# Performance work log

Hardware: AMD Instinct MI355X
Metric: run time of the kernel (lower is better)

## Reference

```python
import jax, jax.numpy as jnp
import numpy as np


def setup_inputs() -> dict:
    key = jax.random.key(0)
    kx, ka = jax.random.split(key)
    B, N, F = 8, 2048, 64
    x = jax.random.normal(kx, (B, N, F), dtype=jnp.float32)
    a = jax.random.uniform(ka, (B, N, N), dtype=jnp.float32)  # adjacency weights in [0,1)
    return {"x": x, "a": a}


def reference(x, a):
    # t[b,i,f] = sum_j a[b,i,j] * x[b,j,f]
    t = jnp.einsum("bij,bjf->bif", a, x)
    # MAX/IND: 1.0 where aggregated signal exceeds 0.5, else 0.0
    # (faithful to tf.where(t>0.5, t/t, t*0.0))
    out = jnp.where(t > 0.5, t / t, t * 0.0)
    return out
```

## Files before the change

kernel.cpp:

```cpp
#include <hip/hip_runtime.h>

#define BATCH 8
#define NROW  2048
#define NF    64
#define JSPLIT 4
#define JPB   (NROW / JSPLIT)
#define CHUNK 32
#define TOT   ((size_t)BATCH * NROW * NF)

typedef float  f32x4  __attribute__((ext_vector_type(4)));
typedef __bf16 bf16x8 __attribute__((ext_vector_type(8)));
typedef unsigned short u16x8 __attribute__((ext_vector_type(8)));

union frag_cast { u16x8 u; bf16x8 b; };

#define AS1 __attribute__((address_space(1)))
#define AS3 __attribute__((address_space(3)))

__device__ __forceinline__ void gld16f(const float* g, float* l) {
  __builtin_amdgcn_global_load_lds((const AS1 void*)g, (AS3 void*)l, 16, 0, 0);
}
__device__ __forceinline__ void gld16u(const unsigned short* g, unsigned short* l) {
  __builtin_amdgcn_global_load_lds((const AS1 void*)g, (AS3 void*)l, 16, 0, 0);
}
__device__ __forceinline__ float ubits(unsigned u) {
  union { unsigned u; float f; } c; c.u = u; return c.f;
}
__device__ __forceinline__ unsigned fbits(float f) {
  union { float f; unsigned u; } c; c.f = f; return c.u;
}

__global__ __launch_bounds__(256, 4)
void prep_x(const float* __restrict__ xg, unsigned short* __restrict__ xs) {
  __shared__ float t[64][65];
  const int b  = blockIdx.y;
  const int j0 = blockIdx.x * 64;
  const int l  = threadIdx.x & 63;
  const int g  = threadIdx.x >> 6;
  const float* src = xg + ((size_t)b * NROW + j0) * NF;
#pragma unroll
  for (int k = 0; k < 16; ++k) {
    const int j = g * 16 + k;
    t[j][l] = src[(size_t)j * NF + l];
  }
  __syncthreads();
#pragma unroll
  for (int k = 0; k < 16; ++k) {
    const int f = g * 16 + k;
    const float v = t[l][f];
    const unsigned u0 = fbits(v);
    const float f0 = ubits(u0 & 0xFFFF0000u);
    const float r  = v - f0;
    const unsigned u1 = fbits(r);
    const float f1 = ubits(u1 & 0xFFFF0000u);
    const float r2 = r - f1;
    const unsigned u2 = fbits(r2);
    const unsigned short s2 =
        (unsigned short)((u2 + 0x7FFFu + ((u2 >> 16) & 1u)) >> 16);
    const size_t o = ((size_t)b * NF + f) * NROW + j0 + l;
    xs[o]           = (unsigned short)(u0 >> 16);
    xs[o + TOT]     = (unsigned short)(u1 >> 16);
    xs[o + 2 * TOT] = s2;
  }
}

__device__ __forceinline__ void split8(const f32x4 q0, const f32x4 q1,
                                       frag_cast* Af) {
  float av[8];
  *(f32x4*)&av[0] = q0;
  *(f32x4*)&av[4] = q1;
  u16x8 h0, h1, h2;
#pragma unroll
  for (int e = 0; e < 8; ++e) {
    const unsigned u0 = fbits(av[e]);
    const float f0 = ubits(u0 & 0xFFFF0000u);
    const float r  = av[e] - f0;
    const unsigned u1 = fbits(r);
    const float f1 = ubits(u1 & 0xFFFF0000u);
    const float r2 = r - f1;
    const unsigned u2 = fbits(r2);
    h0[e] = (unsigned short)(u0 >> 16);
    h1[e] = (unsigned short)(u1 >> 16);
    h2[e] = (unsigned short)((u2 + 0x7FFFu + ((u2 >> 16) & 1u)) >> 16);
  }
  Af[0].u = h0; Af[1].u = h1; Af[2].u = h2;
}

template <bool DIRECT>
__global__ __launch_bounds__(256, 4)
void gemm_mfma(const float* __restrict__ ag, const unsigned short* __restrict__ xs,
               float* __restrict__ outg, float* __restrict__ wp) {
  __shared__ __align__(16) float sA[2][64 * CHUNK];
  __shared__ __align__(16) unsigned short sB[2][3 * 64 * CHUNK];

  const int tid  = threadIdx.x;
  const int ln   = tid & 63;
  const int wv   = tid >> 6;
  const int ln15 = ln & 15;
  const int g    = ln >> 4;
  const int akey = ln15 & 7;
  const int bkey = (ln15 >> 1) & 3;

  const int nwg = gridDim.x * gridDim.y * gridDim.z;
  int flat = blockIdx.x + gridDim.x * (blockIdx.y + gridDim.y * blockIdx.z);
  flat = (flat & 7) * (nwg >> 3) + (flat >> 3);
  const int bx   = flat & 31;
  const int rest = flat >> 5;
  const int z    = DIRECT ? 0 : (rest & 3);
  const int b    = DIRECT ? rest : (rest >> 2);

  const int i0  = bx * 64;
  const int jb  = z * JPB;
  const int nch = (DIRECT ? NROW : JPB) / CHUNK;

  const float* aB = ag + ((size_t)b * NROW + i0) * NROW;
  const unsigned short* xB = xs + (size_t)b * NF * NROW;

  auto stage = [&](int buf, int j0) {
#pragma unroll
    for (int r = 0; r < 2; ++r) {
      const int s   = r * 256 + tid;
      const int row = s >> 3;
      const int q   = (s & 7) ^ (row & 7);
      gld16f(aB + (size_t)row * NROW + j0 + q * 4,
             &sA[buf][0] + (r * 256 + wv * 64) * 4);
    }
#pragma unroll
    for (int lvl = 0; lvl < 3; ++lvl) {
      const int n = tid >> 2;
      const int q = (tid & 3) ^ ((n >> 1) & 3);
      gld16u(xB + (size_t)lvl * TOT + (size_t)n * NROW + j0 + q * 8,
             &sB[buf][0] + (lvl * 256 + wv * 64) * 8);
    }
  };

  double macc[4][4];
#pragma unroll
  for (int i = 0; i < 4; ++i)
#pragma unroll
    for (int j = 0; j < 4; ++j) macc[i][j] = 0.0;

  constexpr int AI[6] = {2, 0, 1, 1, 0, 0};
  constexpr int BI[6] = {0, 2, 1, 0, 1, 0};

  stage(0, jb);

#pragma unroll 1
  for (int t = 0; t < nch; ++t) {
    __syncthreads();
    if (t + 1 < nch) stage((t + 1) & 1, jb + (t + 1) * CHUNK);

    const float* sAb = &sA[t & 1][0];
    const unsigned short* sBb = &sB[t & 1][0];

    const int rowOff = (wv * 16 + ln15) * 32;
    const f32x4 q0 = *(const f32x4*)(sAb + rowOff + (((2 * g)     ^ akey) << 2));
    const f32x4 q1 = *(const f32x4*)(sAb + rowOff + (((2 * g + 1) ^ akey) << 2));
    frag_cast Af[3];
    split8(q0, q1, Af);

    const int bpos = (g ^ bkey) * 8;
    f32x4 c[4];
#pragma unroll
    for (int nt = 0; nt < 4; ++nt) c[nt] = (f32x4){0.f, 0.f, 0.f, 0.f};

#pragma unroll
    for (int ng = 0; ng < 2; ++ng) {
      frag_cast Bv[2][3];
#pragma unroll
      for (int nn = 0; nn < 2; ++nn)
#pragma unroll
        for (int lvl = 0; lvl < 3; ++lvl)
          Bv[nn][lvl].u = *(const u16x8*)(
              sBb + lvl * 2048 + ((ng * 2 + nn) * 16 + ln15) * 32 + bpos);
#pragma unroll
      for (int term = 0; term < 6; ++term)
#pragma unroll
        for (int nn = 0; nn < 2; ++nn) {
          const int nt = ng * 2 + nn;
          c[nt] = __builtin_amdgcn_mfma_f32_16x16x32_bf16(
              Af[AI[term]].b, Bv[nn][BI[term]].b, c[nt], 0, 0, 0);
        }
    }
#pragma unroll
    for (int nt = 0; nt < 4; ++nt) {
      macc[nt][0] += (double)c[nt].x;
      macc[nt][1] += (double)c[nt].y;
      macc[nt][2] += (double)c[nt].z;
      macc[nt][3] += (double)c[nt].w;
    }
  }

  if (DIRECT) {
#pragma unroll
    for (int nt = 0; nt < 4; ++nt)
#pragma unroll
      for (int r = 0; r < 4; ++r)
        outg[((size_t)b * NROW + i0 + wv * 16 + g * 4 + r) * NF + nt * 16 + ln15] =
            (macc[nt][r] > 0.5) ? 1.0f : 0.0f;
  } else {
    float* wb = wp + (size_t)z * TOT;
#pragma unroll
    for (int nt = 0; nt < 4; ++nt)
#pragma unroll
      for (int r = 0; r < 4; ++r)
        wb[((size_t)b * NROW + i0 + wv * 16 + g * 4 + r) * NF + nt * 16 + ln15] =
            (float)macc[nt][r];
  }
}

__global__ __launch_bounds__(256)
void combine_thresh(const float* __restrict__ wsv, float* __restrict__ outg) {
  const size_t e = ((size_t)blockIdx.x * 256 + threadIdx.x) * 4;
  f32x4 p0 = *(const f32x4*)(wsv + e);
  f32x4 p1 = *(const f32x4*)(wsv + e + TOT);
  f32x4 p2 = *(const f32x4*)(wsv + e + 2 * TOT);
  f32x4 p3 = *(const f32x4*)(wsv + e + 3 * TOT);
  f32x4 o;
  o.x = (((double)p0.x + p1.x + p2.x + p3.x) > 0.5) ? 1.0f : 0.0f;
  o.y = (((double)p0.y + p1.y + p2.y + p3.y) > 0.5) ? 1.0f : 0.0f;
  o.z = (((double)p0.z + p1.z + p2.z + p3.z) > 0.5) ? 1.0f : 0.0f;
  o.w = (((double)p0.w + p1.w + p2.w + p3.w) > 0.5) ? 1.0f : 0.0f;
  *(f32x4*)(outg + e) = o;
}

extern "C" void kernel_launch(void* const* d_in, const int* in_sizes, int n_in,
                              void* d_out, int out_size, void* d_ws, size_t ws_size,
                              hipStream_t stream) {
  const float* x = (const float*)d_in[0];
  const float* a = (const float*)d_in[1];
  float* out = (float*)d_out;
  unsigned short* xs = (unsigned short*)d_ws;
  float* wp = (float*)((char*)d_ws + 3 * TOT * sizeof(unsigned short));

  prep_x<<<dim3(NROW / 64, BATCH), dim3(256), 0, stream>>>(x, xs);

  const size_t need = 3 * TOT * sizeof(unsigned short)
                    + (size_t)JSPLIT * TOT * sizeof(float);
  if (ws_size >= need) {
    gemm_mfma<false><<<dim3(NROW / 64, JSPLIT, BATCH), dim3(256), 0, stream>>>(
        a, xs, out, wp);
    combine_thresh<<<dim3((unsigned)(TOT / 1024)), dim3(256), 0, stream>>>(wp, out);
  } else {
    gemm_mfma<true><<<dim3(NROW / 64, 1, BATCH), dim3(256), 0, stream>>>(
        a, xs, out, nullptr);
  }
}
```

Baseline: 47.85 us.

## Switch to 32x32x16 MFMA tiles with 2x2 wave split and flat batch-major grid

```diff
diff --git a/kernel.cpp b/kernel.cpp
--- a/kernel.cpp
+++ b/kernel.cpp
@@ -9,6 +9,7 @@
 #define TOT   ((size_t)BATCH * NROW * NF)
 
 typedef float  f32x4  __attribute__((ext_vector_type(4)));
+typedef float  f32x16 __attribute__((ext_vector_type(16)));
 typedef __bf16 bf16x8 __attribute__((ext_vector_type(8)));
 typedef unsigned short u16x8 __attribute__((ext_vector_type(8)));
 
@@ -93,37 +94,33 @@
   __shared__ __align__(16) float sA[2][64 * CHUNK];
   __shared__ __align__(16) unsigned short sB[2][3 * 64 * CHUNK];
 
-  const int tid  = threadIdx.x;
-  const int ln   = tid & 63;
-  const int wv   = tid >> 6;
-  const int ln15 = ln & 15;
-  const int g    = ln >> 4;
-  const int akey = ln15 & 7;
-  const int bkey = (ln15 >> 1) & 3;
-
-  const int nwg = gridDim.x * gridDim.y * gridDim.z;
-  int flat = blockIdx.x + gridDim.x * (blockIdx.y + gridDim.y * blockIdx.z);
-  flat = (flat & 7) * (nwg >> 3) + (flat >> 3);
-  const int bx   = flat & 31;
-  const int rest = flat >> 5;
-  const int z    = DIRECT ? 0 : (rest & 3);
-  const int b    = DIRECT ? rest : (rest >> 2);
-
-  const int i0  = bx * 64;
-  const int jb  = z * JPB;
-  const int nch = (DIRECT ? NROW : JPB) / CHUNK;
+  const int tid   = threadIdx.x;
+  const int ln    = tid & 63;
+  const int wv    = tid >> 6;
+  const int l31   = ln & 31;
+  const int h     = ln >> 5;
+  const int rhalf = wv & 1;
+  const int chalf = wv >> 1;
+
+  const int flat = blockIdx.x;
+  const int b    = flat & 7;
+  const int bx   = (flat >> 3) & 31;
+  const int z    = DIRECT ? 0 : (flat >> 8);
+  const int i0   = bx * 64;
+  const int jb   = z * JPB;
+  const int nch  = (DIRECT ? NROW : JPB) / CHUNK;
 
   const float* aB = ag + ((size_t)b * NROW + i0) * NROW;
   const unsigned short* xB = xs + (size_t)b * NF * NROW;
 
   auto stage = [&](int buf, int j0) {
 #pragma unroll
-    for (int r = 0; r < 2; ++r) {
-      const int s   = r * 256 + tid;
+    for (int i = 0; i < 2; ++i) {
+      const int s   = i * 256 + tid;
       const int row = s >> 3;
       const int q   = (s & 7) ^ (row & 7);
       gld16f(aB + (size_t)row * NROW + j0 + q * 4,
-             &sA[buf][0] + (r * 256 + wv * 64) * 4);
+             &sA[buf][0] + (i * 256 + wv * 64) * 4);
     }
 #pragma unroll
     for (int lvl = 0; lvl < 3; ++lvl) {
@@ -134,14 +131,17 @@
     }
   };
 
-  double macc[4][4];
-#pragma unroll
-  for (int i = 0; i < 4; ++i)
-#pragma unroll
-    for (int j = 0; j < 4; ++j) macc[i][j] = 0.0;
+  double macc[16];
+#pragma unroll
+  for (int i = 0; i < 16; ++i) macc[i] = 0.0;
 
   constexpr int AI[6] = {2, 0, 1, 1, 0, 0};
   constexpr int BI[6] = {0, 2, 1, 0, 1, 0};
+
+  const int arow = rhalf * 32 + l31;
+  const int akey = l31 & 7;
+  const int ncol = chalf * 32 + l31;
+  const int bkey = (l31 >> 1) & 3;
 
   stage(0, jb);
 
@@ -153,59 +153,48 @@
     const float* sAb = &sA[t & 1][0];
     const unsigned short* sBb = &sB[t & 1][0];
 
-    const int rowOff = (wv * 16 + ln15) * 32;
-    const f32x4 q0 = *(const f32x4*)(sAb + rowOff + (((2 * g)     ^ akey) << 2));
-    const f32x4 q1 = *(const f32x4*)(sAb + rowOff + (((2 * g + 1) ^ akey) << 2));
-    frag_cast Af[3];
-    split8(q0, q1, Af);
-
-    const int bpos = (g ^ bkey) * 8;
-    f32x4 c[4];
-#pragma unroll
-    for (int nt = 0; nt < 4; ++nt) c[nt] = (f32x4){0.f, 0.f, 0.f, 0.f};
-
-#pragma unroll
-    for (int ng = 0; ng < 2; ++ng) {
-      frag_cast Bv[2][3];
-#pragma unroll
-      for (int nn = 0; nn < 2; ++nn)
-#pragma unroll
-        for (int lvl = 0; lvl < 3; ++lvl)
-          Bv[nn][lvl].u = *(const u16x8*)(
-              sBb + lvl * 2048 + ((ng * 2 + nn) * 16 + ln15) * 32 + bpos);
+    f32x16 c;
+#pragma unroll
+    for (int i = 0; i < 16; ++i) c[i] = 0.f;
+
+#pragma unroll
+    for (int sub = 0; sub < 2; ++sub) {
+      const int p0 = (4 * sub + 2 * h)     ^ akey;
+      const int p1 = (4 * sub + 2 * h + 1) ^ akey;
+      const f32x4 q0 = *(const f32x4*)(sAb + arow * 32 + p0 * 4);
+      const f32x4 q1 = *(const f32x4*)(sAb + arow * 32 + p1 * 4);
+      frag_cast Af[3];
+      split8(q0, q1, Af);
+
+      const int bq = (2 * sub + h) ^ bkey;
+      frag_cast Bv[3];
+#pragma unroll
+      for (int lvl = 0; lvl < 3; ++lvl)
+        Bv[lvl].u = *(const u16x8*)(sBb + lvl * 2048 + ncol * 32 + bq * 8);
+
 #pragma unroll
       for (int term = 0; term < 6; ++term)
-#pragma unroll
-        for (int nn = 0; nn < 2; ++nn) {
-          const int nt = ng * 2 + nn;
-          c[nt] = __builtin_amdgcn_mfma_f32_16x16x32_bf16(
-              Af[AI[term]].b, Bv[nn][BI[term]].b, c[nt], 0, 0, 0);
-        }
-    }
-#pragma unroll
-    for (int nt = 0; nt < 4; ++nt) {
-      macc[nt][0] += (double)c[nt].x;
-      macc[nt][1] += (double)c[nt].y;
-      macc[nt][2] += (double)c[nt].z;
-      macc[nt][3] += (double)c[nt].w;
-    }
+        c = __builtin_amdgcn_mfma_f32_32x32x16_bf16(
+            Af[AI[term]].b, Bv[BI[term]].b, c, 0, 0, 0);
+    }
+#pragma unroll
+    for (int i = 0; i < 16; ++i) macc[i] += (double)c[i];
   }
 
   if (DIRECT) {
 #pragma unroll
-    for (int nt = 0; nt < 4; ++nt)
-#pragma unroll
-      for (int r = 0; r < 4; ++r)
-        outg[((size_t)b * NROW + i0 + wv * 16 + g * 4 + r) * NF + nt * 16 + ln15] =
-            (macc[nt][r] > 0.5) ? 1.0f : 0.0f;
+    for (int reg = 0; reg < 16; ++reg) {
+      const int row = i0 + rhalf * 32 + (reg & 3) + 8 * (reg >> 2) + 4 * h;
+      outg[((size_t)b * NROW + row) * NF + chalf * 32 + l31] =
+          (macc[reg] > 0.5) ? 1.0f : 0.0f;
+    }
   } else {
     float* wb = wp + (size_t)z * TOT;
 #pragma unroll
-    for (int nt = 0; nt < 4; ++nt)
-#pragma unroll
-      for (int r = 0; r < 4; ++r)
-        wb[((size_t)b * NROW + i0 + wv * 16 + g * 4 + r) * NF + nt * 16 + ln15] =
-            (float)macc[nt][r];
+    for (int reg = 0; reg < 16; ++reg) {
+      const int row = i0 + rhalf * 32 + (reg & 3) + 8 * (reg >> 2) + 4 * h;
+      wb[((size_t)b * NROW + row) * NF + chalf * 32 + l31] = (float)macc[reg];
+    }
   }
 }
 
@@ -238,11 +227,11 @@
   const size_t need = 3 * TOT * sizeof(unsigned short)
                     + (size_t)JSPLIT * TOT * sizeof(float);
   if (ws_size >= need) {
-    gemm_mfma<false><<<dim3(NROW / 64, JSPLIT, BATCH), dim3(256), 0, stream>>>(
+    gemm_mfma<false><<<dim3(JSPLIT * BATCH * (NROW / 64)), dim3(256), 0, stream>>>(
         a, xs, out, wp);
     combine_thresh<<<dim3((unsigned)(TOT / 1024)), dim3(256), 0, stream>>>(wp, out);
   } else {
-    gemm_mfma<true><<<dim3(NROW / 64, 1, BATCH), dim3(256), 0, stream>>>(
+    gemm_mfma<true><<<dim3(BATCH * (NROW / 64)), dim3(256), 0, stream>>>(
         a, xs, out, nullptr);
   }
 }
```

Measured after the change: 53.31 us. +11.4%, slower.

## Load A directly into registers with two-deep prefetch instead of LDS staging

Applied to the files above, without the earlier changes.

```diff
diff --git a/kernel.cpp b/kernel.cpp
--- a/kernel.cpp
+++ b/kernel.cpp
@@ -17,9 +17,6 @@
 #define AS1 __attribute__((address_space(1)))
 #define AS3 __attribute__((address_space(3)))
 
-__device__ __forceinline__ void gld16f(const float* g, float* l) {
-  __builtin_amdgcn_global_load_lds((const AS1 void*)g, (AS3 void*)l, 16, 0, 0);
-}
 __device__ __forceinline__ void gld16u(const unsigned short* g, unsigned short* l) {
   __builtin_amdgcn_global_load_lds((const AS1 void*)g, (AS3 void*)l, 16, 0, 0);
 }
@@ -90,7 +87,6 @@
 __global__ __launch_bounds__(256, 4)
 void gemm_mfma(const float* __restrict__ ag, const unsigned short* __restrict__ xs,
                float* __restrict__ outg, float* __restrict__ wp) {
-  __shared__ __align__(16) float sA[2][64 * CHUNK];
   __shared__ __align__(16) unsigned short sB[2][3 * 64 * CHUNK];
 
   const int tid  = threadIdx.x;
@@ -98,33 +94,22 @@
   const int wv   = tid >> 6;
   const int ln15 = ln & 15;
   const int g    = ln >> 4;
-  const int akey = ln15 & 7;
   const int bkey = (ln15 >> 1) & 3;
 
-  const int nwg = gridDim.x * gridDim.y * gridDim.z;
-  int flat = blockIdx.x + gridDim.x * (blockIdx.y + gridDim.y * blockIdx.z);
-  flat = (flat & 7) * (nwg >> 3) + (flat >> 3);
-  const int bx   = flat & 31;
-  const int rest = flat >> 5;
-  const int z    = DIRECT ? 0 : (rest & 3);
-  const int b    = DIRECT ? rest : (rest >> 2);
-
-  const int i0  = bx * 64;
-  const int jb  = z * JPB;
-  const int nch = (DIRECT ? NROW : JPB) / CHUNK;
-
-  const float* aB = ag + ((size_t)b * NROW + i0) * NROW;
+  const int flat = blockIdx.x;
+  const int b    = flat & 7;
+  const int rr   = flat >> 3;
+  const int bx   = rr & 31;
+  const int z    = DIRECT ? 0 : ((rr >> 5) & 3);
+  const int i0   = bx * 64;
+  const int jb   = z * JPB;
+  const int nch  = (DIRECT ? NROW : JPB) / CHUNK;
+
+  const float* aA =
+      ag + ((size_t)b * NROW + i0 + wv * 16 + ln15) * NROW + jb + g * 8;
   const unsigned short* xB = xs + (size_t)b * NF * NROW;
 
-  auto stage = [&](int buf, int j0) {
-#pragma unroll
-    for (int r = 0; r < 2; ++r) {
-      const int s   = r * 256 + tid;
-      const int row = s >> 3;
-      const int q   = (s & 7) ^ (row & 7);
-      gld16f(aB + (size_t)row * NROW + j0 + q * 4,
-             &sA[buf][0] + (r * 256 + wv * 64) * 4);
-    }
+  auto stageB = [&](int buf, int j0) {
 #pragma unroll
     for (int lvl = 0; lvl < 3; ++lvl) {
       const int n = tid >> 2;
@@ -143,23 +128,27 @@
   constexpr int AI[6] = {2, 0, 1, 1, 0, 0};
   constexpr int BI[6] = {0, 2, 1, 0, 1, 0};
 
-  stage(0, jb);
-
-#pragma unroll 1
-  for (int t = 0; t < nch; ++t) {
-    __syncthreads();
-    if (t + 1 < nch) stage((t + 1) & 1, jb + (t + 1) * CHUNK);
-
-    const float* sAb = &sA[t & 1][0];
+  stageB(0, jb);
+  f32x4 Aa0 = *(const f32x4*)(aA);
+  f32x4 Aa1 = *(const f32x4*)(aA + 4);
+  f32x4 Ab0 = *(const f32x4*)(aA + CHUNK);
+  f32x4 Ab1 = *(const f32x4*)(aA + CHUNK + 4);
+
+  auto body = [&](int t, f32x4& Ar0, f32x4& Ar1) {
+    asm volatile("s_waitcnt vmcnt(2)" ::: "memory");
+    __builtin_amdgcn_s_barrier();
+    __builtin_amdgcn_sched_barrier(0);
+
+    const int tn = (t + 1 < nch) ? (t + 1) : (nch - 1);
+    stageB((t + 1) & 1, jb + tn * CHUNK);
+
+    frag_cast Af[3];
+    split8(Ar0, Ar1, Af);
+    const int tn2 = (t + 2 < nch) ? (t + 2) : (nch - 1);
+    Ar0 = *(const f32x4*)(aA + (size_t)tn2 * CHUNK);
+    Ar1 = *(const f32x4*)(aA + (size_t)tn2 * CHUNK + 4);
+
     const unsigned short* sBb = &sB[t & 1][0];
-
-    const int rowOff = (wv * 16 + ln15) * 32;
-    const f32x4 q0 = *(const f32x4*)(sAb + rowOff + (((2 * g)     ^ akey) << 2));
-    const f32x4 q1 = *(const f32x4*)(sAb + rowOff + (((2 * g + 1) ^ akey) << 2));
-    frag_cast Af[3];
-    split8(q0, q1, Af);
-
-    const int bpos = (g ^ bkey) * 8;
     f32x4 c[4];
 #pragma unroll
     for (int nt = 0; nt < 4; ++nt) c[nt] = (f32x4){0.f, 0.f, 0.f, 0.f};
@@ -168,11 +157,13 @@
     for (int ng = 0; ng < 2; ++ng) {
       frag_cast Bv[2][3];
 #pragma unroll
-      for (int nn = 0; nn < 2; ++nn)
+      for (int nn = 0; nn < 2; ++nn) {
+        const int ncol = (ng * 2 + nn) * 16 + ln15;
+        const int bq   = g ^ bkey;
 #pragma unroll
         for (int lvl = 0; lvl < 3; ++lvl)
-          Bv[nn][lvl].u = *(const u16x8*)(
-              sBb + lvl * 2048 + ((ng * 2 + nn) * 16 + ln15) * 32 + bpos);
+          Bv[nn][lvl].u = *(const u16x8*)(sBb + lvl * 2048 + ncol * 32 + bq * 8);
+      }
 #pragma unroll
       for (int term = 0; term < 6; ++term)
 #pragma unroll
@@ -189,6 +180,12 @@
       macc[nt][2] += (double)c[nt].z;
       macc[nt][3] += (double)c[nt].w;
     }
+  };
+
+#pragma unroll 1
+  for (int t = 0; t < nch; t += 2) {
+    body(t, Aa0, Aa1);
+    body(t + 1, Ab0, Ab1);
   }
 
   if (DIRECT) {
@@ -238,11 +235,11 @@
   const size_t need = 3 * TOT * sizeof(unsigned short)
                     + (size_t)JSPLIT * TOT * sizeof(float);
   if (ws_size >= need) {
-    gemm_mfma<false><<<dim3(NROW / 64, JSPLIT, BATCH), dim3(256), 0, stream>>>(
+    gemm_mfma<false><<<dim3(JSPLIT * BATCH * (NROW / 64)), dim3(256), 0, stream>>>(
         a, xs, out, wp);
     combine_thresh<<<dim3((unsigned)(TOT / 1024)), dim3(256), 0, stream>>>(wp, out);
   } else {
-    gemm_mfma<true><<<dim3(NROW / 64, 1, BATCH), dim3(256), 0, stream>>>(
+    gemm_mfma<true><<<dim3(BATCH * (NROW / 64)), dim3(256), 0, stream>>>(
         a, xs, out, nullptr);
   }
 }
```

After: 47.68 us. No clear change (-0.3%).
